# Performance work log

Hardware: AMD Instinct MI355X
Metric: run time of the kernel (lower is better)

The kernel has to match this reference:

```python
import jax, jax.numpy as jnp
import numpy as np
from math import factorial

# ---------- Clebsch-Gordan coefficients (e3nn real-basis convention) ----------
def _su2_cg(j1, m1, j2, m2, j3, m3):
    if m3 != m1 + m2:
        return 0.0
    f = factorial
    vmin = int(max(-j1 + j2 + m3, -j1 + m1, 0))
    vmax = int(min(j2 + j3 + m1, j3 - j1 + j2, j3 + m3))
    c = ((2 * j3 + 1) * f(j3 + j1 - j2) * f(j3 - j1 + j2) * f(j1 + j2 - j3) / f(j1 + j2 + j3 + 1)
         * f(j3 + m3) * f(j3 - m3) / (f(j1 + m1) * f(j1 - m1) * f(j2 + m2) * f(j2 - m2))) ** 0.5
    s = 0.0
    for v in range(vmin, vmax + 1):
        s += (-1.0) ** (v + j2 + m2) / f(v) * f(j2 + j3 + m1 - v) * f(j1 - m1 + v) \
             / f(j3 - j1 + j2 - v) / f(j3 + m3 - v) / f(v + j1 - j2 - m3)
    return c * s

def _q(l):
    # change of basis real -> complex spherical harmonics, with (-i)^l phase (e3nn)
    q = np.zeros((2 * l + 1, 2 * l + 1), dtype=np.complex128)
    for m in range(-l, 0):
        q[l + m, l + abs(m)] = 2 ** -0.5
        q[l + m, l - abs(m)] = -1j * 2 ** -0.5
    q[l, l] = 1.0
    for m in range(1, l + 1):
        q[l + m, l + abs(m)] = (-1) ** m * 2 ** -0.5
        q[l + m, l - abs(m)] = 1j * (-1) ** m * 2 ** -0.5
    return (-1j) ** l * q

def _w3j(l1, l2, l3):
    # real-basis Wigner 3j, unit Frobenius norm (e3nn convention)
    C = np.zeros((2 * l1 + 1, 2 * l2 + 1, 2 * l3 + 1), dtype=np.complex128)
    for m1 in range(-l1, l1 + 1):
        for m2 in range(-l2, l2 + 1):
            m3 = m1 + m2
            if abs(m3) <= l3:
                C[l1 + m1, l2 + m2, l3 + m3] = _su2_cg(l1, m1, l2, m2, l3, m3)
    C = np.einsum('ij,kl,mn,ikm->jln', _q(l1), _q(l2), np.conj(_q(l3)), C).real
    return (C / np.linalg.norm(C)).astype(np.float32)

MAX_ELL = 3
AVG_NEIGH = 16.0
P_ENV = 6
N_NODES = 2048
MUL = 64

# tensor-product paths (l1 from Y=0e+1o+2e+3o, l2 from V=0e+1o+2e),
# filtered to ir_out in {0e,1o,2e} (= '0e' + output_irreps), grouped by output ir
PATHS_0E = [(0, 0, 0), (1, 1, 0), (2, 2, 0)]
PATHS_1O = [(0, 1, 1), (1, 0, 1), (1, 2, 1), (2, 1, 1), (3, 2, 1)]
PATHS_2E = [(0, 2, 2), (1, 1, 2), (2, 0, 2), (2, 2, 2), (3, 1, 2)]
_CG = {p: _w3j(*p) for p in PATHS_0E + PATHS_1O + PATHS_2E}
_CG_REC = [_w3j(1, 1, 2), _w3j(2, 1, 3)]  # for SH recursion

def _sh_scales():
    # component normalization: ||Y_l(n)|| = sqrt(2l+1) for unit n
    n = np.array([0.3, 0.5, 0.81]); n /= np.linalg.norm(n)
    nyzx = np.array([n[1], n[2], n[0]])
    Y = np.sqrt(3.0) * nyzx
    scales = []
    for i, l in enumerate((1, 2)):
        A = np.einsum('i,j,ijk->k', Y, nyzx, _CG_REC[i])
        s = np.sqrt(2 * (l + 1) + 1.0) / np.linalg.norm(A)
        scales.append(np.float32(s))
        Y = A * s
    return scales
_SH_SCALES = _sh_scales()

def _sph(vectors):
    # component-normalized real spherical harmonics l=0..3 (e3nn y,z,x basis)
    n = vectors / jnp.linalg.norm(vectors, axis=-1, keepdims=True)
    nyzx = jnp.stack([n[:, 1], n[:, 2], n[:, 0]], axis=-1)
    Y0 = jnp.ones((vectors.shape[0], 1), vectors.dtype)
    Y1 = np.float32(np.sqrt(3.0)) * nyzx
    Y2 = _SH_SCALES[0] * jnp.einsum('ei,ej,ijk->ek', Y1, nyzx, _CG_REC[0])
    Y3 = _SH_SCALES[1] * jnp.einsum('ei,ej,ijk->ek', Y2, nyzx, _CG_REC[1])
    return jnp.concatenate([Y0, Y1, Y2, Y3], axis=-1)  # (E, 16)

def _compute_silu_c():
    # e3nn normalized activation: silu(z) / sqrt(E[silu(z)^2]), z~N(0,1)
    trapz = getattr(np, 'trapezoid', getattr(np, 'trapz', None))
    z = np.linspace(-12.0, 12.0, 200001)
    phi = np.exp(-z * z / 2) / np.sqrt(2 * np.pi)
    s = z / (1.0 + np.exp(-z))
    return np.float32(1.0 / np.sqrt(trapz(s * s * phi, z)))
_SILU_C = _compute_silu_c()

def _silu_n(x):
    return jax.nn.silu(x) * _SILU_C

def _sl(l):
    return slice(l * l, (l + 1) * (l + 1))

def _envelope(d, p=P_ENV):
    # e3nn poly_envelope(p-1, 2) == DimeNet cutoff polynomial
    a = np.float32(-(p + 1) * (p + 2) / 2)
    b = np.float32(p * (p + 2))
    c = np.float32(-p * (p + 1) / 2)
    val = 1.0 + a * d ** p + b * d ** (p + 1) + c * d ** (p + 2)
    return jnp.where(d < 1.0, val, jnp.zeros_like(d))

def _forward(vectors, x, V, senders, W0, W1, W2, W3, Wl1, Wl2):
    E = x.shape[0]
    # edge-wise channel weights: mlp((mul_gcd,), act=None)
    w = (x @ W0) * np.float32(1.0 / np.sqrt(x.shape[1]))          # (E, MUL)
    Y = _sph(vectors)                                              # (E, 16)
    wY = w[:, :, None] * Y[:, None, :]                             # (E, MUL, 16)
    node_sum = jax.ops.segment_sum(wY, senders, num_segments=N_NODES)
    wY = node_sum[senders] * np.float32(1.0 / np.sqrt(AVG_NEIGH))  # scatter_sum(map_back=True)
    Vc = V.reshape(E, MUL, 9)                                      # mul_to_axis: 0e+1o+2e

    def tp(paths):
        outs = [np.float32(np.sqrt(2 * l3 + 1)) *
                jnp.einsum('eui,euj,ijk->euk', wY[:, :, _sl(l1)], Vc[:, :, _sl(l2)], _CG[(l1, l2, l3)])
                for (l1, l2, l3) in paths]
        return jnp.stack(outs, axis=2)  # (E, MUL, n_paths, 2*l3+1)

    s0 = tp(PATHS_0E).reshape(E, MUL * 3)      # 192x0e scalars
    v1 = tp(PATHS_1O).reshape(E, MUL * 5, 3)   # 320x1o
    v2 = tp(PATHS_2E).reshape(E, MUL * 5, 5)   # 320x2e

    # scalar track: concat 0e outputs, 3-layer MLP (normalized silu, no output act)
    x2 = jnp.concatenate([x, s0], axis=1)
    h = _silu_n(x2 @ W1 * np.float32(1.0 / np.sqrt(x2.shape[1])))
    h = _silu_n(h @ W2 * np.float32(1.0 / np.sqrt(h.shape[1])))
    h = h @ W3 * np.float32(1.0 / np.sqrt(h.shape[1]))
    d = jnp.linalg.norm(vectors, axis=-1, keepdims=True)
    x_out = _envelope(d) * h                                       # (E, 64)

    # equivariant track: e3nn Linear to 64x0e+64x1o+64x2e (no 0e input -> zeros)
    inv = np.float32(1.0 / np.sqrt(MUL * 5))
    o1 = jnp.einsum('emi,mu->eui', v1, Wl1) * inv
    o2 = jnp.einsum('emi,mu->eui', v2, Wl2) * inv
    V_out = jnp.concatenate([jnp.zeros((E, MUL), x.dtype),
                             o1.reshape(E, MUL * 3), o2.reshape(E, MUL * 5)], axis=1)  # (E, 576)
    return x_out, V_out

def setup_inputs() -> dict:
    key = jax.random.key(0)
    ks = jax.random.split(key, 11)
    E, XD = 32768, 128
    v = jax.random.normal(ks[0], (E, 3), dtype=jnp.float32)
    r = jax.random.uniform(ks[1], (E, 1), minval=0.05, maxval=0.95, dtype=jnp.float32)
    vectors = v / jnp.linalg.norm(v, axis=1, keepdims=True) * r  # lengths in (0,1): inside cutoff
    return {
        'vectors': vectors,
        'x': jax.random.normal(ks[2], (E, XD), dtype=jnp.float32),
        'V': jax.random.normal(ks[3], (E, MUL * 9), dtype=jnp.float32),
        'senders': jax.random.randint(ks[4], (E,), 0, N_NODES),
        'W0': jax.random.normal(ks[5], (XD, MUL), dtype=jnp.float32),
        'W1': jax.random.normal(ks[6], (XD + 3 * MUL, 64), dtype=jnp.float32),
        'W2': jax.random.normal(ks[7], (64, 64), dtype=jnp.float32),
        'W3': jax.random.normal(ks[8], (64, 64), dtype=jnp.float32),
        'Wl1': jax.random.normal(ks[9], (5 * MUL, MUL), dtype=jnp.float32),
        'Wl2': jax.random.normal(ks[10], (5 * MUL, MUL), dtype=jnp.float32),
    }

def reference(vectors, x, V, senders, W0, W1, W2, W3, Wl1, Wl2):
    return _forward(vectors, x, V, senders, W0, W1, W2, W3, Wl1, Wl2)
```

## Files before the change

kernel.cpp:

```cpp
#include <hip/hip_runtime.h>
#include <cmath>
#include <utility>

#define DI __device__ __forceinline__

typedef __attribute__((ext_vector_type(8))) short  short8;
typedef __attribute__((ext_vector_type(4))) float  f32x4;

constexpr double cfact(int n){ double r=1.0; for(int i=2;i<=n;++i) r*=(double)i; return r; }
constexpr double csqrt(double x){ if(x<=0.0) return 0.0; double g = x>1.0?x:1.0; for(int i=0;i<100;++i) g = 0.5*(g + x/g); return g; }
constexpr double csgn(int k){ int m = k%2; if(m<0) m+=2; return m? -1.0:1.0; }
constexpr int cmax3(int a,int b,int c){ int m=a>b?a:b; return m>c?m:c; }
constexpr int cmin3(int a,int b,int c){ int m=a<b?a:b; return m<c?m:c; }

struct cplx { double r, i; };
constexpr cplx cmul(cplx a, cplx b){ return cplx{a.r*b.r - a.i*b.i, a.r*b.i + a.i*b.r}; }
constexpr cplx cadd(cplx a, cplx b){ return cplx{a.r+b.r, a.i+b.i}; }
constexpr cplx cscale(cplx a, double s){ return cplx{a.r*s, a.i*s}; }
constexpr cplx cconj(cplx a){ return cplx{a.r, -a.i}; }

constexpr double su2_cg(int j1,int m1,int j2,int m2,int j3,int m3){
  if (m3 != m1+m2) return 0.0;
  const int vmin = cmax3(-j1+j2+m3, -j1+m1, 0);
  const int vmax = cmin3(j2+j3+m1, j3-j1+j2, j3+m3);
  const double c = csqrt((2.0*j3+1.0) * cfact(j3+j1-j2)*cfact(j3-j1+j2)*cfact(j1+j2-j3)/cfact(j1+j2+j3+1)
                         * cfact(j3+m3)*cfact(j3-m3)
                         / (cfact(j1+m1)*cfact(j1-m1)*cfact(j2+m2)*cfact(j2-m2)));
  double s = 0.0;
  for (int v=vmin; v<=vmax; ++v){
    s += csgn(v+j2+m2)/cfact(v)*cfact(j2+j3+m1-v)*cfact(j1-m1+v)
         /cfact(j3-j1+j2-v)/cfact(j3+m3-v)/cfact(v+j1-j2-m3);
  }
  return c*s;
}

template<int L> struct QM { cplx v[2*L+1][2*L+1]; };
template<int L> constexpr QM<L> qmat(){
  QM<L> q{};
  const double is2 = 0.70710678118654752440;
  for (int m=-L; m<0; ++m){
    q.v[L+m][L-m] = cplx{is2, 0.0};
    q.v[L+m][L+m] = cplx{0.0, -is2};
  }
  q.v[L][L] = cplx{1.0, 0.0};
  for (int m=1; m<=L; ++m){
    const double sg = (m%2)? -1.0 : 1.0;
    q.v[L+m][L+m] = cplx{sg*is2, 0.0};
    q.v[L+m][L-m] = cplx{0.0, sg*is2};
  }
  const cplx ph = (L%4==0)?cplx{1,0} : (L%4==1)?cplx{0,-1} : (L%4==2)?cplx{-1,0} : cplx{0,1};
  for (int a=0;a<2*L+1;++a) for(int b=0;b<2*L+1;++b) q.v[a][b] = cmul(ph, q.v[a][b]);
  return q;
}

template<int L1,int L2,int L3> struct W3J { float v[2*L1+1][2*L2+1][2*L3+1]; };

template<int L1,int L2,int L3> constexpr W3J<L1,L2,L3> w3j(){
  constexpr int N1=2*L1+1, N2=2*L2+1, N3=2*L3+1;
  double C[N1][N2][N3] = {};
  for (int m1=-L1;m1<=L1;++m1) for (int m2=-L2;m2<=L2;++m2){
    const int m3=m1+m2;
    if (m3>=-L3 && m3<=L3) C[L1+m1][L2+m2][L3+m3] = su2_cg(L1,m1,L2,m2,L3,m3);
  }
  const QM<L1> q1 = qmat<L1>(); const QM<L2> q2 = qmat<L2>(); const QM<L3> q3 = qmat<L3>();
  cplx T1[N1][N2][N3] = {};
  for(int j=0;j<N1;++j) for(int k=0;k<N2;++k) for(int m=0;m<N3;++m){
    cplx acc{0,0};
    for(int i=0;i<N1;++i) acc = cadd(acc, cscale(q1.v[i][j], C[i][k][m]));
    T1[j][k][m]=acc;
  }
  cplx T2[N1][N2][N3] = {};
  for(int j=0;j<N1;++j) for(int l=0;l<N2;++l) for(int m=0;m<N3;++m){
    cplx acc{0,0};
    for(int k=0;k<N2;++k) acc = cadd(acc, cmul(q2.v[k][l], T1[j][k][m]));
    T2[j][l][m]=acc;
  }
  double O[N1][N2][N3] = {};
  double fro = 0.0;
  for(int j=0;j<N1;++j) for(int l=0;l<N2;++l) for(int n=0;n<N3;++n){
    cplx acc{0,0};
    for(int m=0;m<N3;++m) acc = cadd(acc, cmul(cconj(q3.v[m][n]), T2[j][l][m]));
    O[j][l][n] = acc.r;
    fro += acc.r*acc.r;
  }
  const double inv = 1.0/csqrt(fro);
  W3J<L1,L2,L3> w{};
  for(int j=0;j<N1;++j) for(int l=0;l<N2;++l) for(int n=0;n<N3;++n)
    w.v[j][l][n] = (float)(O[j][l][n]*inv);
  return w;
}

constexpr auto CG_000 = w3j<0,0,0>();
constexpr auto CG_110 = w3j<1,1,0>();
constexpr auto CG_220 = w3j<2,2,0>();
constexpr auto CG_011 = w3j<0,1,1>();
constexpr auto CG_101 = w3j<1,0,1>();
constexpr auto CG_121 = w3j<1,2,1>();
constexpr auto CG_211 = w3j<2,1,1>();
constexpr auto CG_321 = w3j<3,2,1>();
constexpr auto CG_022 = w3j<0,2,2>();
constexpr auto CG_112 = w3j<1,1,2>();
constexpr auto CG_202 = w3j<2,0,2>();
constexpr auto CG_222 = w3j<2,2,2>();
constexpr auto CG_312 = w3j<3,1,2>();
constexpr auto CG_213 = w3j<2,1,3>();

struct ShS { double s0, s1; };
constexpr ShS sh_scales(){
  const double n0=0.3,n1=0.5,n2=0.81;
  const double nn = csqrt(n0*n0+n1*n1+n2*n2);
  const double ny[3] = {n1/nn, n2/nn, n0/nn};
  const double sq3 = csqrt(3.0);
  double Y1[3]; for(int i=0;i<3;++i) Y1[i] = sq3*ny[i];
  double A[5] = {};
  for(int i=0;i<3;++i) for(int j=0;j<3;++j) for(int k=0;k<5;++k)
    A[k] += Y1[i]*ny[j]*(double)CG_112.v[i][j][k];
  double na=0; for(int k=0;k<5;++k) na += A[k]*A[k]; na = csqrt(na);
  const double s0 = csqrt(5.0)/na;
  double Y2[5]; for(int k=0;k<5;++k) Y2[k] = A[k]*s0;
  double B[7] = {};
  for(int i=0;i<5;++i) for(int j=0;j<3;++j) for(int k=0;k<7;++k)
    B[k] += Y2[i]*ny[j]*(double)CG_213.v[i][j][k];
  double nb=0; for(int k=0;k<7;++k) nb += B[k]*B[k]; nb = csqrt(nb);
  const double s1 = csqrt(7.0)/nb;
  return ShS{s0,s1};
}
constexpr ShS SHS = sh_scales();

template<typename F, int... Is>
DI void sfor_impl(F&& f, std::integer_sequence<int, Is...>){ (f(std::integral_constant<int,Is>{}), ...); }
template<int N, typename F>
DI void sfor(F&& f){ sfor_impl(f, std::make_integer_sequence<int, N>{}); }

template<int N>
__host__ __device__ constexpr bool col_any(const float (&c)[N]){
  for(int k=0;k<N;++k) if (c[k]!=0.0f) return true;
  return false;
}

#define CONTRACT3(TAB, NI, NJ, NK, SCALE, INI, INJ, OUT) \
  sfor<(NI)>([&](auto I__){ constexpr int i__ = decltype(I__)::value; \
    sfor<(NJ)>([&](auto J__){ constexpr int j__ = decltype(J__)::value; \
      if constexpr (col_any((TAB).v[i__][j__])) { \
        const float t__ = (INI)[i__] * (INJ)[j__]; \
        sfor<(NK)>([&](auto K__){ constexpr int k__ = decltype(K__)::value; \
          if constexpr ((TAB).v[i__][j__][k__] != 0.0f) { \
            constexpr float c__ = (float)((double)(TAB).v[i__][j__][k__] * (double)(SCALE)); \
            (OUT)[k__] = fmaf(c__, t__, (OUT)[k__]); \
          } }); } }); });

DI unsigned short f2bf(float f){
  unsigned int u = __float_as_uint(f);
  u += 0x7fffu + ((u >> 16) & 1u);
  return (unsigned short)(u >> 16);
}
DI float silu_n(float z, float c){ return c * (z / (1.0f + __expf(-z))); }

constexpr float SQRT3F        = (float)csqrt(3.0);
constexpr double SQ3D         = csqrt(3.0);
constexpr double SQ5D         = csqrt(5.0);
constexpr float INV_SQRT_XD   = (float)(1.0/csqrt(128.0));
constexpr float INV_SQRT_NEI  = 0.25f;
constexpr float INV320        = (float)(1.0/csqrt(320.0));

constexpr int E_TOT = 32768;
constexpr int NNODE = 2048;

DI short8 load_bfrag_raw(const float* __restrict__ W, int kt, int nt, int lane){
  const int q = lane >> 4, c = lane & 15;
  const float* src = W + (kt*32 + q*8)*64 + nt*16 + c;
  short8 b;
  #pragma unroll
  for (int j=0;j<8;++j) b[j] = (short)f2bf(src[j*64]);
  return b;
}

__global__ __launch_bounds__(256) void k_setup(
    const int* __restrict__ senders, int* __restrict__ pos, int* __restrict__ cnt,
    const float* __restrict__ W0, const float* __restrict__ W1,
    const float* __restrict__ Wl1, const float* __restrict__ Wl2,
    short8* __restrict__ bfrag)
{
  const int blk = blockIdx.x;
  if (blk < 34){
    if (bfrag == nullptr) return;
    const int wv = threadIdx.x >> 6, lane = threadIdx.x & 63;
    const int wid = blk*4 + wv;
    if (wid >= 136) return;
    const float* W; int kt, nt;
    if (wid < 16){ W = W0; kt = wid>>2; nt = wid&3; }
    else { const int t = wid-16; const int mat = t/40, r = t%40;
           W = (mat==0)?W1 : (mat==1)?Wl1 : Wl2; kt = r>>2; nt = r&3; }
    bfrag[wid*64 + lane] = load_bfrag_raw(W, kt, nt, lane);
  } else {
    const int e = (blk-34)*256 + threadIdx.x;
    if (e < E_TOT) pos[e] = atomicAdd(&cnt[senders[e]], 1);
  }
}

__global__ __launch_bounds__(256) void k_scan(const int* __restrict__ cnt, int* __restrict__ off)
{
  __shared__ int ts[256];
  const int t = threadIdx.x;
  int loc[8]; int s = 0;
  #pragma unroll
  for (int i=0;i<8;++i){ int v = cnt[t*8+i]; loc[i] = s; s += v; }
  ts[t] = s;
  __syncthreads();
  int val = s;
  for (int d=1; d<256; d<<=1){
    int other = (t>=d)? ts[t-d] : 0;
    __syncthreads();
    val += other; ts[t] = val;
    __syncthreads();
  }
  const int base = val - s;
  #pragma unroll
  for (int i=0;i<8;++i) off[t*8+i] = base + loc[i];
  if (t==255) off[2048] = val;
}

__global__ __launch_bounds__(256) void k_wy(
    const float* __restrict__ vectors, const float* __restrict__ x,
    const int* __restrict__ senders, const float* __restrict__ W0,
    const int* __restrict__ pos, const int* __restrict__ off,
    const short8* __restrict__ bfrag,
    float* __restrict__ w_un, float* __restrict__ Y_un, int* __restrict__ eids)
{
  const int tid = threadIdx.x, lane = tid & 63, wv = tid >> 6;
  const int e0 = blockIdx.x * 64;
  const int r = lane & 15, q = lane >> 4;
  const int erow = e0 + wv*16 + r;

  f32x4 acc[4] = {{0.f,0.f,0.f,0.f},{0.f,0.f,0.f,0.f},{0.f,0.f,0.f,0.f},{0.f,0.f,0.f,0.f}};
  #pragma unroll
  for (int kt=0; kt<4; ++kt){
    const float4* xp = (const float4*)(x + (size_t)erow*128 + kt*32 + q*8);
    const float4 xa = xp[0], xb = xp[1];
    short8 a;
    a[0]=(short)f2bf(xa.x); a[1]=(short)f2bf(xa.y); a[2]=(short)f2bf(xa.z); a[3]=(short)f2bf(xa.w);
    a[4]=(short)f2bf(xb.x); a[5]=(short)f2bf(xb.y); a[6]=(short)f2bf(xb.z); a[7]=(short)f2bf(xb.w);
    #pragma unroll
    for (int nt=0; nt<4; ++nt){
      const short8 b = (bfrag != nullptr) ? bfrag[(kt*4+nt)*64 + lane]
                                          : load_bfrag_raw(W0, kt, nt, lane);
      acc[nt] = __builtin_amdgcn_mfma_f32_16x16x32_bf16(a, b, acc[nt], 0,0,0);
    }
  }
  #pragma unroll
  for (int nt=0; nt<4; ++nt)
    #pragma unroll
    for (int reg=0; reg<4; ++reg){
      const int row = q*4 + reg;
      w_un[(size_t)(e0 + wv*16 + row)*64 + nt*16 + r] = acc[nt][reg] * INV_SQRT_XD;
    }

  if (tid < 64){
    const int e = e0 + tid;
    const float vx = vectors[e*3+0], vy = vectors[e*3+1], vz = vectors[e*3+2];
    const float dn = sqrtf(vx*vx+vy*vy+vz*vz);
    const float ny[3] = {vy/dn, vz/dn, vx/dn};
    float Y[16];
    Y[0] = 1.f; Y[1] = SQRT3F*ny[0]; Y[2] = SQRT3F*ny[1]; Y[3] = SQRT3F*ny[2];
    #pragma unroll
    for (int k=4;k<16;++k) Y[k] = 0.f;
    CONTRACT3(CG_112, 3,3,5, SHS.s0, (Y+1), ny, (Y+4));
    CONTRACT3(CG_213, 5,3,7, SHS.s1, (Y+4), ny, (Y+9));
    #pragma unroll
    for (int k=0;k<16;++k) Y_un[e*16+k] = Y[k];
    const int s = senders[e];
    eids[off[s] + pos[e]] = e;
  }
}

__global__ __launch_bounds__(256) void k_gather(
    const float* __restrict__ w_un, const float* __restrict__ Y_un,
    const int* __restrict__ off, const int* __restrict__ eids,
    float* __restrict__ node_sum)
{
  const int lane = threadIdx.x & 63;
  const int wv = threadIdx.x >> 6;
  const int n = __builtin_amdgcn_readfirstlane((int)blockIdx.x*4 + wv);
  const int p0 = off[n], p1 = off[n+1];
  float acc[16];
  #pragma unroll
  for (int k=0;k<16;++k) acc[k] = 0.f;
  for (int p=p0; p<p1; ++p){
    const int eid = eids[p];
    const float wu = w_un[(size_t)eid*64 + lane];
    const float* yr = Y_un + eid*16;
    #pragma unroll
    for (int k=0;k<16;++k) acc[k] = fmaf(yr[k], wu, acc[k]);
  }
  float* dst = node_sum + n*1024;
  #pragma unroll
  for (int k=0;k<16;++k) dst[k*64 + lane] = acc[k] * INV_SQRT_NEI;
}

DI void wr2(char* AF, int tile, int row, int m, float val){
  const int kt = m >> 5, m0 = m & 31;
  *(unsigned short*)(AF + (((tile*10 + kt)*16 + row)<<6) + (m0<<1)) = f2bf(val);
}

__global__ __launch_bounds__(256,4) void k_main(
    const float* __restrict__ vectors, const float* __restrict__ x,
    const float* __restrict__ V, const int* __restrict__ senders,
    const float* __restrict__ W1, const float* __restrict__ W2,
    const float* __restrict__ W3, const float* __restrict__ Wl1,
    const float* __restrict__ Wl2, const float* __restrict__ node_sum,
    const short8* __restrict__ bfrag,
    float* __restrict__ out_x, float* __restrict__ out_V, float silu_c)
{
  __shared__ __align__(16) char smem[40960];
  char*  AF    = smem;
  float* h1s   = (float*)smem;
  float* h2s   = (float*)(smem + 1024);
  float* stage = (float*)(smem + 2048);

  const int tid  = threadIdx.x;
  const int lane = tid & 63;
  const int wv   = tid >> 6;
  const int blk  = blockIdx.x;

  {
    const int el = wv;
    const int e  = __builtin_amdgcn_readfirstlane(blk*4 + el);
    const int s  = senders[e];
    const int u  = lane;

    float* smV = (float*)(smem + wv*2304);
    #pragma unroll
    for (int j=0;j<9;++j) smV[j*64 + lane] = V[(size_t)e*576 + j*64 + lane];
    float vc[9];
    #pragma unroll
    for (int j=0;j<9;++j) vc[j] = smV[u*9 + j];

    float g[16];
    const float* nsrow = node_sum + s*1024;
    #pragma unroll
    for (int k=0;k<16;++k) g[k] = nsrow[k*64+u];
    const float x0 = x[(size_t)e*128 + u];
    const float x1 = x[(size_t)e*128 + 64 + u];

    __syncthreads();

    float s0[3] = {0.f,0.f,0.f};
    float v1o[5][3] = {};
    float v2o[5][5] = {};
    CONTRACT3(CG_000, 1,1,1, 1.0, (g+0), (vc+0), (&s0[0]));
    CONTRACT3(CG_110, 3,3,1, 1.0, (g+1), (vc+1), (&s0[1]));
    CONTRACT3(CG_220, 5,5,1, 1.0, (g+4), (vc+4), (&s0[2]));
    CONTRACT3(CG_011, 1,3,3, SQ3D, (g+0), (vc+1), (v1o[0]));
    CONTRACT3(CG_101, 3,1,3, SQ3D, (g+1), (vc+0), (v1o[1]));
    CONTRACT3(CG_121, 3,5,3, SQ3D, (g+1), (vc+4), (v1o[2]));
    CONTRACT3(CG_211, 5,3,3, SQ3D, (g+4), (vc+1), (v1o[3]));
    CONTRACT3(CG_321, 7,5,3, SQ3D, (g+9), (vc+4), (v1o[4]));
    CONTRACT3(CG_022, 1,5,5, SQ5D, (g+0), (vc+4), (v2o[0]));
    CONTRACT3(CG_112, 3,3,5, SQ5D, (g+1), (vc+1), (v2o[1]));
    CONTRACT3(CG_202, 5,1,5, SQ5D, (g+4), (vc+0), (v2o[2]));
    CONTRACT3(CG_222, 5,5,5, SQ5D, (g+4), (vc+4), (v2o[3]));
    CONTRACT3(CG_312, 7,3,5, SQ5D, (g+9), (vc+1), (v2o[4]));

    wr2(AF, 0, el, u,      x0);
    wr2(AF, 0, el, 64 + u, x1);
    #pragma unroll
    for (int p=0;p<3;++p) wr2(AF, 0, el, 128 + u*3 + p, s0[p]);
    #pragma unroll
    for (int p=0;p<5;++p){
      const int m = u*5 + p;
      #pragma unroll
      for (int i=0;i<3;++i){ const int rr = i*4+el; wr2(AF, 1, rr, m, v1o[p][i]); }
      #pragma unroll
      for (int i=0;i<5;++i){ const int rr = i*4+el; wr2(AF, 2+(rr>>4), rr&15, m, v2o[p][i]); }
    }
  }
  __syncthreads();

  f32x4 acc0={0.f,0.f,0.f,0.f}, acc1=acc0, acc2=acc0, acc3=acc0;
  const int nt = wv;
  const int aoff = (lane&15)*64 + (lane>>4)*16;
  for (int kt=0; kt<10; ++kt){
    short8 b0, b1, b2;
    if (bfrag != nullptr){
      b0 = bfrag[(16 + kt*4 + nt)*64 + lane];
      b1 = bfrag[(56 + kt*4 + nt)*64 + lane];
      b2 = bfrag[(96 + kt*4 + nt)*64 + lane];
    } else {
      b0 = load_bfrag_raw(W1,  kt, nt, lane);
      b1 = load_bfrag_raw(Wl1, kt, nt, lane);
      b2 = load_bfrag_raw(Wl2, kt, nt, lane);
    }
    const char* ab = AF + kt*1024 + aoff;
    const short8 a0 = *(const short8*)(ab);
    const short8 a1 = *(const short8*)(ab + 10240);
    const short8 a2 = *(const short8*)(ab + 20480);
    const short8 a3 = *(const short8*)(ab + 30720);
    acc0 = __builtin_amdgcn_mfma_f32_16x16x32_bf16(a0, b0, acc0, 0,0,0);
    acc1 = __builtin_amdgcn_mfma_f32_16x16x32_bf16(a1, b1, acc1, 0,0,0);
    acc2 = __builtin_amdgcn_mfma_f32_16x16x32_bf16(a2, b2, acc2, 0,0,0);
    acc3 = __builtin_amdgcn_mfma_f32_16x16x32_bf16(a3, b2, acc3, 0,0,0);
  }
  __syncthreads();

  const int col = lane & 15, qq = lane >> 4;
  const int u2 = nt*16 + col;
  stage[qq*576 + u2] = 0.f;
  #pragma unroll
  for (int reg=0; reg<4; ++reg){
    const int row = qq*4 + reg;
    if (row < 4) h1s[row*64 + u2] = silu_n(acc0[reg] * INV320, silu_c);
    if (row < 12){ const int i = row>>2, ee = row&3;
      stage[ee*576 + 64 + u2*3 + i] = acc1[reg] * INV320; }
    { const int i2 = row>>2, ee = row&3;
      stage[ee*576 + 256 + u2*5 + i2] = acc2[reg] * INV320; }
    if (row < 4){
      stage[row*576 + 256 + u2*5 + 4] = acc3[reg] * INV320; }
  }
  __syncthreads();

  const int e2 = blk*4 + wv;
  float sacc = 0.f;
  #pragma unroll 8
  for (int c=0;c<64;++c) sacc = fmaf(h1s[wv*64+c], W2[c*64+lane], sacc);
  h2s[wv*64 + lane] = silu_n(sacc * 0.125f, silu_c);
  __syncthreads();

  const float vx = vectors[e2*3+0], vy = vectors[e2*3+1], vz = vectors[e2*3+2];
  const float d  = sqrtf(vx*vx + vy*vy + vz*vz);
  const float d3 = d*d*d;
  const float d6 = d3*d3;
  const float env = (d < 1.f) ? (1.f + d6*(-28.f + d*(48.f + d*(-21.f)))) : 0.f;
  float sacc2 = 0.f;
  #pragma unroll 8
  for (int c=0;c<64;++c) sacc2 = fmaf(h2s[wv*64+c], W3[c*64+lane], sacc2);
  out_x[(size_t)e2*64 + lane] = env * (sacc2 * 0.125f);

  const float* st = stage + wv*576;
  #pragma unroll
  for (int j=0;j<9;++j) out_V[(size_t)e2*576 + j*64 + lane] = st[j*64 + lane];
}

static const float g_silu_c = [](){
  const int N = 200001;
  const double h = 24.0/(double)(N-1);
  double acc = 0.0;
  for (int i=0;i<N;++i){
    const double z = -12.0 + h*(double)i;
    const double phi = std::exp(-z*z/2.0)/std::sqrt(2.0*M_PI);
    const double s = z/(1.0+std::exp(-z));
    const double f = s*s*phi;
    acc += (i==0 || i==N-1) ? 0.5*f : f;
  }
  return (float)(1.0/std::sqrt(acc*h));
}();

extern "C" void kernel_launch(void* const* d_in, const int* in_sizes, int n_in,
                              void* d_out, int out_size, void* d_ws, size_t ws_size,
                              hipStream_t stream) {
  (void)in_sizes; (void)n_in; (void)out_size;
  const float* vectors = (const float*)d_in[0];
  const float* x       = (const float*)d_in[1];
  const float* V       = (const float*)d_in[2];
  const int*   senders = (const int*)  d_in[3];
  const float* W0      = (const float*)d_in[4];
  const float* W1      = (const float*)d_in[5];
  const float* W2      = (const float*)d_in[6];
  const float* W3      = (const float*)d_in[7];
  const float* Wl1     = (const float*)d_in[8];
  const float* Wl2     = (const float*)d_in[9];
  float* out_x = (float*)d_out;
  float* out_V = out_x + (size_t)E_TOT*64;

  char* ob = (char*)d_out;
  int*   pos   = (int*)(ob);
  int*   cnt   = (int*)(ob + 131072);
  int*   off   = (int*)(ob + 139264);
  int*   eids  = (int*)(ob + 151552);
  float* w_un  = (float*)(ob + 282624);
  float* Y_un  = (float*)(ob + 282624 + 8388608);

  float* node_sum = (float*)d_ws;
  const size_t WS_NEED = (size_t)8*1024*1024 + 136*1024;
  short8* bfrag = (ws_size >= WS_NEED) ? (short8*)((char*)d_ws + 8*1024*1024) : nullptr;

  hipMemsetAsync(cnt, 0, 8192, stream);
  k_setup <<<dim3(162), dim3(256), 0, stream>>>(senders, pos, cnt, W0, W1, Wl1, Wl2, bfrag);
  k_scan  <<<dim3(1),   dim3(256), 0, stream>>>(cnt, off);
  k_wy    <<<dim3(E_TOT/64), dim3(256), 0, stream>>>(vectors, x, senders, W0, pos, off, bfrag, w_un, Y_un, eids);
  k_gather<<<dim3(NNODE/4),  dim3(256), 0, stream>>>(w_un, Y_un, off, eids, node_sum);
  k_main  <<<dim3(E_TOT/4),  dim3(256), 0, stream>>>(vectors, x, V, senders,
                                                     W1, W2, W3, Wl1, Wl2,
                                                     node_sum, bfrag, out_x, out_V, g_silu_c);
}
```

Baseline: 275.8 us.

## Pack A tiles into three, swizzle LDS, raise occupancy, prefetch gather loads

Packs the scalar and vector-1o rows of the A operand into a single 16-row tile, so the MFMA stage uses three A tiles instead of four and shared memory drops from 40 KB to 30 KB. This allows raising the launch bound to 5 blocks per CU. An XOR swizzle is added to the A-tile LDS layout, and the stage stride is padded to 580, both to reduce bank conflicts. The gather kernel software-pipelines edge loads one iteration ahead to hide memory latency, at the cost of extra registers.

```diff
diff --git a/kernel.cpp b/kernel.cpp
--- a/kernel.cpp
+++ b/kernel.cpp
@@ -285,12 +285,26 @@
   float acc[16];
   #pragma unroll
   for (int k=0;k<16;++k) acc[k] = 0.f;
-  for (int p=p0; p<p1; ++p){
-    const int eid = eids[p];
-    const float wu = w_un[(size_t)eid*64 + lane];
-    const float* yr = Y_un + eid*16;
-    #pragma unroll
-    for (int k=0;k<16;++k) acc[k] = fmaf(yr[k], wu, acc[k]);
+  if (p1 > p0){
+    int eid = eids[p0];
+    float wu = w_un[(size_t)eid*64 + lane];
+    float yv[16];
+    #pragma unroll
+    for (int k=0;k<16;++k) yv[k] = Y_un[eid*16 + k];
+    for (int p=p0+1; p<p1; ++p){
+      const int eid2 = eids[p];
+      const float wu2 = w_un[(size_t)eid2*64 + lane];
+      float yv2[16];
+      #pragma unroll
+      for (int k=0;k<16;++k) yv2[k] = Y_un[eid2*16 + k];
+      #pragma unroll
+      for (int k=0;k<16;++k) acc[k] = fmaf(yv[k], wu, acc[k]);
+      wu = wu2;
+      #pragma unroll
+      for (int k=0;k<16;++k) yv[k] = yv2[k];
+    }
+    #pragma unroll
+    for (int k=0;k<16;++k) acc[k] = fmaf(yv[k], wu, acc[k]);
   }
   float* dst = node_sum + n*1024;
   #pragma unroll
@@ -299,10 +313,13 @@
 
 DI void wr2(char* AF, int tile, int row, int m, float val){
   const int kt = m >> 5, m0 = m & 31;
-  *(unsigned short*)(AF + (((tile*10 + kt)*16 + row)<<6) + (m0<<1)) = f2bf(val);
-}
-
-__global__ __launch_bounds__(256,4) void k_main(
+  *(unsigned short*)(AF + (((tile*10 + kt)*16 + row)<<6)
+                        + ((m0<<1) ^ (((row>>1)&3)<<4))) = f2bf(val);
+}
+
+constexpr int SSTR = 580;
+
+__global__ __launch_bounds__(256,5) void k_main(
     const float* __restrict__ vectors, const float* __restrict__ x,
     const float* __restrict__ V, const int* __restrict__ senders,
     const float* __restrict__ W1, const float* __restrict__ W2,
@@ -311,7 +328,7 @@
     const short8* __restrict__ bfrag,
     float* __restrict__ out_x, float* __restrict__ out_V, float silu_c)
 {
-  __shared__ __align__(16) char smem[40960];
+  __shared__ __align__(16) char smem[30720];
   char*  AF    = smem;
   float* h1s   = (float*)smem;
   float* h2s   = (float*)(smem + 1024);
@@ -369,16 +386,19 @@
     for (int p=0;p<5;++p){
       const int m = u*5 + p;
       #pragma unroll
-      for (int i=0;i<3;++i){ const int rr = i*4+el; wr2(AF, 1, rr, m, v1o[p][i]); }
+      for (int i=0;i<3;++i) wr2(AF, 0, 4 + i*4 + el, m, v1o[p][i]);
       #pragma unroll
-      for (int i=0;i<5;++i){ const int rr = i*4+el; wr2(AF, 2+(rr>>4), rr&15, m, v2o[p][i]); }
+      for (int i=0;i<4;++i) wr2(AF, 1, i*4 + el, m, v2o[p][i]);
+      wr2(AF, 2, el, m, v2o[p][4]);
     }
   }
   __syncthreads();
 
-  f32x4 acc0={0.f,0.f,0.f,0.f}, acc1=acc0, acc2=acc0, acc3=acc0;
+  f32x4 accS={0.f,0.f,0.f,0.f}, accV1=accS, accA=accS, accB=accS;
   const int nt = wv;
-  const int aoff = (lane&15)*64 + (lane>>4)*16;
+  const int arow = lane & 15;
+  const int aoff = arow*64 + (((lane>>4)<<4) ^ (((arow>>1)&3)<<4));
+  #pragma unroll 2
   for (int kt=0; kt<10; ++kt){
     short8 b0, b1, b2;
     if (bfrag != nullptr){
@@ -394,27 +414,28 @@
     const short8 a0 = *(const short8*)(ab);
     const short8 a1 = *(const short8*)(ab + 10240);
     const short8 a2 = *(const short8*)(ab + 20480);
-    const short8 a3 = *(const short8*)(ab + 30720);
-    acc0 = __builtin_amdgcn_mfma_f32_16x16x32_bf16(a0, b0, acc0, 0,0,0);
-    acc1 = __builtin_amdgcn_mfma_f32_16x16x32_bf16(a1, b1, acc1, 0,0,0);
-    acc2 = __builtin_amdgcn_mfma_f32_16x16x32_bf16(a2, b2, acc2, 0,0,0);
-    acc3 = __builtin_amdgcn_mfma_f32_16x16x32_bf16(a3, b2, acc3, 0,0,0);
+    accS  = __builtin_amdgcn_mfma_f32_16x16x32_bf16(a0, b0, accS,  0,0,0);
+    accV1 = __builtin_amdgcn_mfma_f32_16x16x32_bf16(a0, b1, accV1, 0,0,0);
+    accA  = __builtin_amdgcn_mfma_f32_16x16x32_bf16(a1, b2, accA,  0,0,0);
+    accB  = __builtin_amdgcn_mfma_f32_16x16x32_bf16(a2, b2, accB,  0,0,0);
   }
   __syncthreads();
 
   const int col = lane & 15, qq = lane >> 4;
   const int u2 = nt*16 + col;
-  stage[qq*576 + u2] = 0.f;
+  stage[qq*SSTR + u2] = 0.f;
   #pragma unroll
   for (int reg=0; reg<4; ++reg){
     const int row = qq*4 + reg;
-    if (row < 4) h1s[row*64 + u2] = silu_n(acc0[reg] * INV320, silu_c);
-    if (row < 12){ const int i = row>>2, ee = row&3;
-      stage[ee*576 + 64 + u2*3 + i] = acc1[reg] * INV320; }
+    if (row < 4){
+      h1s[row*64 + u2] = silu_n(accS[reg] * INV320, silu_c);
+      stage[row*SSTR + 256 + u2*5 + 4] = accB[reg] * INV320;
+    } else {
+      const int rr = row - 4, i = rr>>2, ee = rr&3;
+      stage[ee*SSTR + 64 + u2*3 + i] = accV1[reg] * INV320;
+    }
     { const int i2 = row>>2, ee = row&3;
-      stage[ee*576 + 256 + u2*5 + i2] = acc2[reg] * INV320; }
-    if (row < 4){
-      stage[row*576 + 256 + u2*5 + 4] = acc3[reg] * INV320; }
+      stage[ee*SSTR + 256 + u2*5 + i2] = accA[reg] * INV320; }
   }
   __syncthreads();
 
@@ -435,7 +456,7 @@
   for (int c=0;c<64;++c) sacc2 = fmaf(h2s[wv*64+c], W3[c*64+lane], sacc2);
   out_x[(size_t)e2*64 + lane] = env * (sacc2 * 0.125f);
 
-  const float* st = stage + wv*576;
+  const float* st = stage + wv*SSTR;
   #pragma unroll
   for (int j=0;j<9;++j) out_V[(size_t)e2*576 + j*64 + lane] = st[j*64 + lane];
 }
```

After: 272.7 us. No clear change (-1.1%).
